# Performance work log

Measured on AMD Instinct MI355X. Metric: run time of the kernel, lower is better.

The kernel has to match this reference:

```python
import jax, jax.numpy as jnp
import numpy as np

EMB, HEADS, LEVELS, POINTS = 256, 8, 4, 4
DHEAD = EMB // HEADS
SHAPES = [(128, 128), (64, 64), (32, 32), (16, 16)]  # (H, W) per level
S = sum(h * w for h, w in SHAPES)  # 21760 flattened multiscale tokens
B, Q = 2, S
LN_EPS = 1e-5


def setup_inputs() -> dict:
    key = jax.random.key(0)
    ks = jax.random.split(key, 10)
    f = lambda k, shp, s=0.02: jax.random.normal(k, shp, jnp.float32) * s
    return {
        "img_feat": jax.random.normal(ks[0], (B, S, EMB), jnp.float32),
        "img_shapes": jnp.array(SHAPES, jnp.int32),
        "img_mask": jnp.zeros((B, S), bool),  # True = padded
        "img_valid_ratios": jnp.ones((B, LEVELS, 2), jnp.float32),
        "query_feat": jax.random.normal(ks[1], (B, Q, EMB), jnp.float32),
        "query_pos": jax.random.normal(ks[2], (B, Q, EMB), jnp.float32),
        "query_points": jax.random.uniform(ks[3], (B, Q, 2), jnp.float32),
        "W_value": f(ks[4], (EMB, EMB)), "b_value": jnp.zeros((EMB,), jnp.float32),
        "W_off": f(ks[5], (EMB, HEADS * LEVELS * POINTS * 2)),
        "b_off": f(ks[6], (HEADS * LEVELS * POINTS * 2,), 0.5),
        "W_attn": f(ks[7], (EMB, HEADS * LEVELS * POINTS)),
        "b_attn": jnp.zeros((HEADS * LEVELS * POINTS,), jnp.float32),
        "W_out": f(ks[8], (EMB, EMB)), "b_out": jnp.zeros((EMB,), jnp.float32),
        "ln_gamma": jnp.ones((EMB,), jnp.float32), "ln_beta": jnp.zeros((EMB,), jnp.float32),
    }


def reference(img_feat, img_shapes, img_mask, img_valid_ratios, query_feat, query_pos,
              query_points, W_value, b_value, W_off, b_off, W_attn, b_attn, W_out, b_out,
              ln_gamma, ln_beta):
    Bq, Qn = query_feat.shape[:2]
    # value projection + padding mask, split heads: [B, S, H, D]
    v = img_feat @ W_value + b_value
    v = jnp.where(img_mask[:, :, None], 0.0, v).reshape(Bq, -1, HEADS, DHEAD)
    q = query_feat + query_pos  # position-modulated query
    off = (q @ W_off + b_off).reshape(Bq, Qn, HEADS, LEVELS, POINTS, 2)
    attn = jax.nn.softmax((q @ W_attn + b_attn).reshape(Bq, Qn, HEADS, LEVELS * POINTS), -1)
    attn = attn.reshape(Bq, Qn, HEADS, LEVELS, POINTS)
    # reference points scaled by per-level valid ratios: [B, Q, L, 2] (x, y in [0,1])
    ref = query_points[:, :, None, :] * img_valid_ratios[:, None, :, :]
    bb = jnp.arange(Bq)[:, None, None, None]
    hh = jnp.arange(HEADS)[None, None, :, None]
    out = jnp.zeros((Bq, Qn, HEADS, DHEAD), q.dtype)
    start = 0
    for l, (H, W) in enumerate(SHAPES):
        norm = jnp.array([W, H], q.dtype)
        loc = ref[:, :, None, l, None, :] + off[:, :, :, l] / norm  # [B,Q,H,P,2]
        # grid_sample align_corners=False pixel coords
        x = loc[..., 0] * W - 0.5
        y = loc[..., 1] * H - 0.5
        x0 = jnp.floor(x); y0 = jnp.floor(y)
        wx = x - x0; wy = y - y0
        x0i = x0.astype(jnp.int32); y0i = y0.astype(jnp.int32)
        samp = jnp.zeros((Bq, Qn, HEADS, POINTS, DHEAD), q.dtype)
        for dx, dy, w in ((0, 0, (1 - wx) * (1 - wy)), (1, 0, wx * (1 - wy)),
                          (0, 1, (1 - wx) * wy), (1, 1, wx * wy)):
            xi = x0i + dx; yi = y0i + dy
            ok = (xi >= 0) & (xi < W) & (yi >= 0) & (yi < H)  # zero padding
            idx = start + jnp.clip(yi, 0, H - 1) * W + jnp.clip(xi, 0, W - 1)
            samp = samp + (w * ok)[..., None] * v[bb, idx, hh, :]
        out = out + jnp.einsum('bqhp,bqhpd->bqhd', attn[:, :, :, l], samp)
        start += H * W
    update = out.reshape(Bq, Qn, EMB) @ W_out + b_out
    # SkipConnection: LayerNorm(skip + dropout(update)), dropout p=0
    x = query_feat + update
    mu = x.mean(-1, keepdims=True)
    var = ((x - mu) ** 2).mean(-1, keepdims=True)
    return (x - mu) * jax.lax.rsqrt(var + LN_EPS) * ln_gamma + ln_beta
```

## Files before the change

kernel.cpp:

```cpp
#include <hip/hip_runtime.h>
#include <hip/hip_bf16.h>

#define EMB 256
#define SEQ 21760
#define NB 2
#define NROW (NB * SEQ)
#define LN_EPS 1e-5f

typedef __hip_bfloat16 bf16;
typedef short bf16x8 __attribute__((ext_vector_type(8)));
typedef float f32x4 __attribute__((ext_vector_type(4)));

__device__ __forceinline__ unsigned short f2bf(float f) {
  __hip_bfloat16 h = __float2bfloat16(f);
  return *reinterpret_cast<unsigned short*>(&h);
}
__device__ __forceinline__ float bf2f(unsigned short u) {
  return __uint_as_float((unsigned int)u << 16);
}
__device__ __forceinline__ float bflo(unsigned int u) { return __uint_as_float(u << 16); }
__device__ __forceinline__ float bfhi(unsigned int u) { return __uint_as_float(u & 0xffff0000u); }

#if defined(__has_builtin)
#if __has_builtin(__builtin_amdgcn_fdot2_f32_bf16)
#define USE_DOT2 1
#endif
#endif
#ifdef USE_DOT2
__device__ __forceinline__ float dot2bf(unsigned int a, unsigned int b, float c) {
  float d;
  asm("v_dot2_f32_bf16 %0, %1, %2, %3" : "=v"(d) : "v"(a), "v"(b), "v"(c));
  return d;
}
#endif

__global__ __launch_bounds__(256) void k_trans_all(const float* __restrict__ Wv,
                                                   const float* __restrict__ Woff,
                                                   const float* __restrict__ Wattn,
                                                   const float* __restrict__ Wout,
                                                   unsigned short* __restrict__ WvT,
                                                   unsigned short* __restrict__ WcatT,
                                                   unsigned short* __restrict__ WoutT) {
  const int bid = blockIdx.x, k = threadIdx.x;
  if (bid < 256) {
    WvT[bid * 256 + k] = f2bf(Wv[k * 256 + bid]);
  } else if (bid < 512) {
    const int n = bid - 256;
    WcatT[n * 256 + k] = f2bf(Woff[k * 256 + n]);
  } else if (bid < 640) {
    const int n = bid - 512;
    WcatT[(256 + n) * 256 + k] = f2bf(Wattn[k * 128 + n]);
  } else {
    const int n = bid - 640;
    WoutT[n * 256 + k] = f2bf(Wout[k * 256 + n]);
  }
}

__global__ __launch_bounds__(256) void k_value(const float* __restrict__ A,
                                               const unsigned short* __restrict__ Wt,
                                               const float* __restrict__ bias,
                                               const unsigned char* __restrict__ mask,
                                               bf16* __restrict__ V) {
  __shared__ unsigned short As[64 * 256];
  const int tid = threadIdx.x;
  const int lane = tid & 63, w = tid >> 6;
  const int row0 = blockIdx.x * 64;
#pragma unroll
  for (int it = 0; it < 8; ++it) {
    const int cid = it * 256 + tid;
    const int row = cid >> 5, c = cid & 31;
    const float4* p = (const float4*)(A + (size_t)(row0 + row) * 256 + c * 8);
    const float4 a0 = p[0], a1 = p[1];
    union { unsigned short u[8]; uint4 q; } pk;
    pk.u[0] = f2bf(a0.x); pk.u[1] = f2bf(a0.y); pk.u[2] = f2bf(a0.z); pk.u[3] = f2bf(a0.w);
    pk.u[4] = f2bf(a1.x); pk.u[5] = f2bf(a1.y); pk.u[6] = f2bf(a1.z); pk.u[7] = f2bf(a1.w);
    *(uint4*)((char*)As + row * 512 + ((c * 16) ^ ((row & 7) << 4))) = pk.q;
  }
  __syncthreads();
  const int lg16 = lane >> 4, l16 = lane & 15;
  f32x4 acc[4][4] = {};
#pragma unroll
  for (int kk = 0; kk < 8; ++kk) {
    bf16x8 af[4], bh[4];
#pragma unroll
    for (int mf = 0; mf < 4; ++mf) {
      const int row = mf * 16 + l16;
      af[mf] = *(const bf16x8*)((const char*)As + row * 512 +
                                ((kk * 64 + lg16 * 16) ^ ((row & 7) << 4)));
    }
#pragma unroll
    for (int nf = 0; nf < 4; ++nf) {
      const int col = w * 64 + nf * 16 + l16;
      bh[nf] = *(const bf16x8*)(Wt + (size_t)col * 256 + kk * 32 + lg16 * 8);
    }
#pragma unroll
    for (int mf = 0; mf < 4; ++mf)
#pragma unroll
      for (int nf = 0; nf < 4; ++nf)
        acc[mf][nf] = __builtin_amdgcn_mfma_f32_16x16x32_bf16(af[mf], bh[nf], acc[mf][nf], 0, 0, 0);
  }
#pragma unroll
  for (int mf = 0; mf < 4; ++mf) {
    const int rbase = mf * 16 + lg16 * 4;
    const uchar4 mk = *(const uchar4*)(mask + row0 + rbase);
#pragma unroll
    for (int nf = 0; nf < 4; ++nf) {
      const int col = w * 64 + nf * 16 + l16;
      const int hh = col >> 5, ch = col & 31;
      const float bb = bias[col];
#pragma unroll
      for (int r = 0; r < 4; ++r) {
        const unsigned char m = (r == 0) ? mk.x : (r == 1) ? mk.y : (r == 2) ? mk.z : mk.w;
        const float v = m ? 0.f : (acc[mf][nf][r] + bb);
        V[(size_t)hh * (NROW * 32) + (size_t)(row0 + rbase + r) * 32 + ch] =
            __float2bfloat16(v);
      }
    }
  }
}

__global__ __launch_bounds__(256) void k_offattn(const float* __restrict__ qf,
                                                 const float* __restrict__ qp,
                                                 const unsigned short* __restrict__ Wt,
                                                 const float* __restrict__ boff,
                                                 const float* __restrict__ battn,
                                                 bf16* __restrict__ off,
                                                 bf16* __restrict__ lg) {
  __shared__ unsigned short As[64 * 256];
  const int tid = threadIdx.x;
  const int lane = tid & 63, w = tid >> 6;
  const int row0 = blockIdx.x * 64;
#pragma unroll
  for (int it = 0; it < 8; ++it) {
    const int cid = it * 256 + tid;
    const int row = cid >> 5, c = cid & 31;
    const float4* pf = (const float4*)(qf + (size_t)(row0 + row) * 256 + c * 8);
    const float4* pp = (const float4*)(qp + (size_t)(row0 + row) * 256 + c * 8);
    const float4 a0 = pf[0], a1 = pf[1], b0 = pp[0], b1 = pp[1];
    union { unsigned short u[8]; uint4 q; } pk;
    pk.u[0] = f2bf(a0.x + b0.x); pk.u[1] = f2bf(a0.y + b0.y);
    pk.u[2] = f2bf(a0.z + b0.z); pk.u[3] = f2bf(a0.w + b0.w);
    pk.u[4] = f2bf(a1.x + b1.x); pk.u[5] = f2bf(a1.y + b1.y);
    pk.u[6] = f2bf(a1.z + b1.z); pk.u[7] = f2bf(a1.w + b1.w);
    *(uint4*)((char*)As + row * 512 + ((c * 16) ^ ((row & 7) << 4))) = pk.q;
  }
  __syncthreads();
  const int lg16 = lane >> 4, l16 = lane & 15;
  f32x4 acc[4][6] = {};
#pragma unroll
  for (int kk = 0; kk < 8; ++kk) {
    bf16x8 af[4], bh[6];
#pragma unroll
    for (int mf = 0; mf < 4; ++mf) {
      const int row = mf * 16 + l16;
      af[mf] = *(const bf16x8*)((const char*)As + row * 512 +
                                ((kk * 64 + lg16 * 16) ^ ((row & 7) << 4)));
    }
#pragma unroll
    for (int nf = 0; nf < 6; ++nf) {
      const int col = w * 96 + nf * 16 + l16;
      bh[nf] = *(const bf16x8*)(Wt + (size_t)col * 256 + kk * 32 + lg16 * 8);
    }
#pragma unroll
    for (int mf = 0; mf < 4; ++mf)
#pragma unroll
      for (int nf = 0; nf < 6; ++nf)
        acc[mf][nf] = __builtin_amdgcn_mfma_f32_16x16x32_bf16(af[mf], bh[nf], acc[mf][nf], 0, 0, 0);
  }
#pragma unroll
  for (int mf = 0; mf < 4; ++mf) {
    const int rbase = row0 + mf * 16 + lg16 * 4;
#pragma unroll
    for (int nf = 0; nf < 6; ++nf) {
      const int col = w * 96 + nf * 16 + l16;
      if (col < 256) {
        const float bb = boff[col];
#pragma unroll
        for (int r = 0; r < 4; ++r)
          off[(size_t)(rbase + r) * 256 + col] = __float2bfloat16(acc[mf][nf][r] + bb);
      } else {
        const float bb = battn[col - 256];
#pragma unroll
        for (int r = 0; r < 4; ++r)
          lg[(size_t)(rbase + r) * 128 + (col - 256)] = __float2bfloat16(acc[mf][nf][r] + bb);
      }
    }
  }
}

__global__ __launch_bounds__(256) void k_sample(const bf16* __restrict__ V,
                                                const bf16* __restrict__ off,
                                                const bf16* __restrict__ lg,
                                                const float* __restrict__ qpts,
                                                const float* __restrict__ vratio,
                                                unsigned short* __restrict__ samp) {
  __shared__ uint4 sIdx[64 * 17];
  __shared__ uint2 sW[64 * 17];
  __shared__ float sMax[64], sInv[64];
  const int t = threadIdx.x;
  const int h = blockIdx.x & 7;
  const int row0 = (blockIdx.x >> 3) * 64;

  if (t < 64) {
    const int row = row0 + t;
    const uint4* lp = (const uint4*)(lg + (size_t)row * 128 + h * 16);
    uint4 u0 = lp[0], u1 = lp[1];
    float v[16];
    v[0] = bflo(u0.x); v[1] = bfhi(u0.x); v[2] = bflo(u0.y); v[3] = bfhi(u0.y);
    v[4] = bflo(u0.z); v[5] = bfhi(u0.z); v[6] = bflo(u0.w); v[7] = bfhi(u0.w);
    v[8] = bflo(u1.x); v[9] = bfhi(u1.x); v[10] = bflo(u1.y); v[11] = bfhi(u1.y);
    v[12] = bflo(u1.z); v[13] = bfhi(u1.z); v[14] = bflo(u1.w); v[15] = bfhi(u1.w);
    float m = v[0];
#pragma unroll
    for (int i = 1; i < 16; ++i) m = fmaxf(m, v[i]);
    float s = 0.f;
#pragma unroll
    for (int i = 0; i < 16; ++i) s += __expf(v[i] - m);
    sMax[t] = m;
    sInv[t] = 1.f / s;
  }
  __syncthreads();

  const int Wl_[4] = {128, 64, 32, 16};
  const int st_[4] = {0, 16384, 20480, 21504};
#pragma unroll
  for (int tt = 0; tt < 4; ++tt) {
    const int sid = t + tt * 256;
    const int q = sid >> 4, i = sid & 15, l = i >> 2;
    const int row = row0 + q;
    const int b = row >= SEQ;
    const unsigned int u = *(const unsigned int*)(off + (size_t)row * 256 + (h * 16 + i) * 2);
    const float ox = bflo(u), oy = bfhi(u);
    const float lgv = bf2f(*(const unsigned short*)(lg + (size_t)row * 128 + h * 16 + i));
    const float e = __expf(lgv - sMax[q]) * sInv[q];
    const float px = qpts[(size_t)row * 2], py = qpts[(size_t)row * 2 + 1];
    const float vrx = vratio[b * 8 + l * 2], vry = vratio[b * 8 + l * 2 + 1];
    const int Wl = Wl_[l];
    const float fW = (float)Wl;
    const float x = fmaf(px * vrx, fW, ox) - 0.5f;
    const float y = fmaf(py * vry, fW, oy) - 0.5f;
    const float fx = floorf(x), fy = floorf(y);
    const float wx = x - fx, wy = y - fy;
    const int x0 = (int)fx, y0 = (int)fy;
    const int x1 = x0 + 1, y1 = y0 + 1;
    const int xc0 = min(max(x0, 0), Wl - 1), xc1 = min(max(x1, 0), Wl - 1);
    const int yc0 = min(max(y0, 0), Wl - 1), yc1 = min(max(y1, 0), Wl - 1);
    const float ox0 = (x0 >= 0 && x0 < Wl) ? e : 0.f;
    const float ox1 = (x1 >= 0 && x1 < Wl) ? e : 0.f;
    const float oy0 = (y0 >= 0 && y0 < Wl) ? 1.f : 0.f;
    const float oy1 = (y1 >= 0 && y1 < Wl) ? 1.f : 0.f;
    const int base = b * SEQ + st_[l];
    const int r0 = base + yc0 * Wl, r1 = base + yc1 * Wl;
    uint4 I4;
    I4.x = (unsigned int)(r0 + xc0) << 6;
    I4.y = (unsigned int)(r0 + xc1) << 6;
    I4.z = (unsigned int)(r1 + xc0) << 6;
    I4.w = (unsigned int)(r1 + xc1) << 6;
    uint2 Wp;
    Wp.x = (unsigned int)f2bf((1.f - wx) * (1.f - wy) * ox0 * oy0) |
           ((unsigned int)f2bf(wx * (1.f - wy) * ox1 * oy0) << 16);
    Wp.y = (unsigned int)f2bf((1.f - wx) * wy * ox0 * oy1) |
           ((unsigned int)f2bf(wx * wy * ox1 * oy1) << 16);
    sIdx[q * 17 + i] = I4;
    sW[q * 17 + i] = Wp;
  }
  __syncthreads();

  const int q = t >> 2, dg = t & 3;
  const int row = row0 + q;
  const char* vbase = (const char*)(V + (size_t)h * (NROW * 32)) + dg * 16;
  float a0 = 0.f, a1 = 0.f, a2 = 0.f, a3 = 0.f;
  float a4 = 0.f, a5 = 0.f, a6 = 0.f, a7 = 0.f;
#pragma unroll
  for (int i = 0; i < 16; ++i) {
    const uint4 I4 = sIdx[q * 17 + i];
    const uint2 Wp = sW[q * 17 + i];
    const uint4 Au = *(const uint4*)(vbase + I4.x);
    const uint4 Bu = *(const uint4*)(vbase + I4.y);
    const uint4 Cu = *(const uint4*)(vbase + I4.z);
    const uint4 Du = *(const uint4*)(vbase + I4.w);
#ifdef USE_DOT2
    a0 = dot2bf(__builtin_amdgcn_perm(Bu.x, Au.x, 0x05040100u), Wp.x, a0);
    a1 = dot2bf(__builtin_amdgcn_perm(Bu.x, Au.x, 0x07060302u), Wp.x, a1);
    a2 = dot2bf(__builtin_amdgcn_perm(Bu.y, Au.y, 0x05040100u), Wp.x, a2);
    a3 = dot2bf(__builtin_amdgcn_perm(Bu.y, Au.y, 0x07060302u), Wp.x, a3);
    a4 = dot2bf(__builtin_amdgcn_perm(Bu.z, Au.z, 0x05040100u), Wp.x, a4);
    a5 = dot2bf(__builtin_amdgcn_perm(Bu.z, Au.z, 0x07060302u), Wp.x, a5);
    a6 = dot2bf(__builtin_amdgcn_perm(Bu.w, Au.w, 0x05040100u), Wp.x, a6);
    a7 = dot2bf(__builtin_amdgcn_perm(Bu.w, Au.w, 0x07060302u), Wp.x, a7);
    a0 = dot2bf(__builtin_amdgcn_perm(Du.x, Cu.x, 0x05040100u), Wp.y, a0);
    a1 = dot2bf(__builtin_amdgcn_perm(Du.x, Cu.x, 0x07060302u), Wp.y, a1);
    a2 = dot2bf(__builtin_amdgcn_perm(Du.y, Cu.y, 0x05040100u), Wp.y, a2);
    a3 = dot2bf(__builtin_amdgcn_perm(Du.y, Cu.y, 0x07060302u), Wp.y, a3);
    a4 = dot2bf(__builtin_amdgcn_perm(Du.z, Cu.z, 0x05040100u), Wp.y, a4);
    a5 = dot2bf(__builtin_amdgcn_perm(Du.z, Cu.z, 0x07060302u), Wp.y, a5);
    a6 = dot2bf(__builtin_amdgcn_perm(Du.w, Cu.w, 0x05040100u), Wp.y, a6);
    a7 = dot2bf(__builtin_amdgcn_perm(Du.w, Cu.w, 0x07060302u), Wp.y, a7);
#else
    {
      const float w0 = bflo(Wp.x), w1 = bfhi(Wp.x);
      const float w2 = bflo(Wp.y), w3 = bfhi(Wp.y);
      a0 = fmaf(w0, bflo(Au.x), a0); a1 = fmaf(w0, bfhi(Au.x), a1);
      a2 = fmaf(w0, bflo(Au.y), a2); a3 = fmaf(w0, bfhi(Au.y), a3);
      a4 = fmaf(w0, bflo(Au.z), a4); a5 = fmaf(w0, bfhi(Au.z), a5);
      a6 = fmaf(w0, bflo(Au.w), a6); a7 = fmaf(w0, bfhi(Au.w), a7);
      a0 = fmaf(w1, bflo(Bu.x), a0); a1 = fmaf(w1, bfhi(Bu.x), a1);
      a2 = fmaf(w1, bflo(Bu.y), a2); a3 = fmaf(w1, bfhi(Bu.y), a3);
      a4 = fmaf(w1, bflo(Bu.z), a4); a5 = fmaf(w1, bfhi(Bu.z), a5);
      a6 = fmaf(w1, bflo(Bu.w), a6); a7 = fmaf(w1, bfhi(Bu.w), a7);
      a0 = fmaf(w2, bflo(Cu.x), a0); a1 = fmaf(w2, bfhi(Cu.x), a1);
      a2 = fmaf(w2, bflo(Cu.y), a2); a3 = fmaf(w2, bfhi(Cu.y), a3);
      a4 = fmaf(w2, bflo(Cu.z), a4); a5 = fmaf(w2, bfhi(Cu.z), a5);
      a6 = fmaf(w2, bflo(Cu.w), a6); a7 = fmaf(w2, bfhi(Cu.w), a7);
      a0 = fmaf(w3, bflo(Du.x), a0); a1 = fmaf(w3, bfhi(Du.x), a1);
      a2 = fmaf(w3, bflo(Du.y), a2); a3 = fmaf(w3, bfhi(Du.y), a3);
      a4 = fmaf(w3, bflo(Du.z), a4); a5 = fmaf(w3, bfhi(Du.z), a5);
      a6 = fmaf(w3, bflo(Du.w), a6); a7 = fmaf(w3, bfhi(Du.w), a7);
    }
#endif
  }
  uint4 pk;
  pk.x = (unsigned int)f2bf(a0) | ((unsigned int)f2bf(a1) << 16);
  pk.y = (unsigned int)f2bf(a2) | ((unsigned int)f2bf(a3) << 16);
  pk.z = (unsigned int)f2bf(a4) | ((unsigned int)f2bf(a5) << 16);
  pk.w = (unsigned int)f2bf(a6) | ((unsigned int)f2bf(a7) << 16);
  *(uint4*)((char*)samp + (size_t)row * 512 + (h * 32 + dg * 8) * 2) = pk;
}

__global__ __launch_bounds__(256) void k_upd(const unsigned short* __restrict__ A,
                                             const unsigned short* __restrict__ Wt,
                                             const float* __restrict__ bias,
                                             bf16* __restrict__ U) {
  __shared__ unsigned short As[64 * 256];
  const int tid = threadIdx.x;
  const int lane = tid & 63, w = tid >> 6;
  const int row0 = blockIdx.x * 64;
#pragma unroll
  for (int it = 0; it < 8; ++it) {
    const int cid = it * 256 + tid;
    const int row = cid >> 5, c = cid & 31;
    const uint4 q = *(const uint4*)(A + (size_t)(row0 + row) * 256 + c * 8);
    *(uint4*)((char*)As + row * 512 + ((c * 16) ^ ((row & 7) << 4))) = q;
  }
  __syncthreads();
  const int lg16 = lane >> 4, l16 = lane & 15;
  f32x4 acc[4][4] = {};
#pragma unroll
  for (int kk = 0; kk < 8; ++kk) {
    bf16x8 af[4], bh[4];
#pragma unroll
    for (int mf = 0; mf < 4; ++mf) {
      const int row = mf * 16 + l16;
      af[mf] = *(const bf16x8*)((const char*)As + row * 512 +
                                ((kk * 64 + lg16 * 16) ^ ((row & 7) << 4)));
    }
#pragma unroll
    for (int nf = 0; nf < 4; ++nf) {
      const int col = w * 64 + nf * 16 + l16;
      bh[nf] = *(const bf16x8*)(Wt + (size_t)col * 256 + kk * 32 + lg16 * 8);
    }
#pragma unroll
    for (int mf = 0; mf < 4; ++mf)
#pragma unroll
      for (int nf = 0; nf < 4; ++nf)
        acc[mf][nf] = __builtin_amdgcn_mfma_f32_16x16x32_bf16(af[mf], bh[nf], acc[mf][nf], 0, 0, 0);
  }
#pragma unroll
  for (int mf = 0; mf < 4; ++mf) {
    const int rbase = row0 + mf * 16 + lg16 * 4;
#pragma unroll
    for (int nf = 0; nf < 4; ++nf) {
      const int col = w * 64 + nf * 16 + l16;
      const float bb = bias[col];
#pragma unroll
      for (int r = 0; r < 4; ++r)
        U[(size_t)(rbase + r) * 256 + col] = __float2bfloat16(acc[mf][nf][r] + bb);
    }
  }
}

__global__ __launch_bounds__(256) void k_ln(const unsigned short* __restrict__ upd,
                                            const float* __restrict__ qf,
                                            const float* __restrict__ gamma,
                                            const float* __restrict__ beta,
                                            float* __restrict__ y) {
  const int w = threadIdx.x >> 6, lane = threadIdx.x & 63;
  const int row = blockIdx.x * 4 + w;
  const int c = lane * 4;
  const ushort4 u = *(const ushort4*)(upd + (size_t)row * 256 + c);
  const float4 qv = *(const float4*)(qf + (size_t)row * 256 + c);
  const float x0 = qv.x + bf2f(u.x);
  const float x1 = qv.y + bf2f(u.y);
  const float x2 = qv.z + bf2f(u.z);
  const float x3 = qv.w + bf2f(u.w);
  float s1 = x0 + x1 + x2 + x3;
  float s2 = x0 * x0 + x1 * x1 + x2 * x2 + x3 * x3;
#pragma unroll
  for (int o = 32; o >= 1; o >>= 1) {
    s1 += __shfl_xor(s1, o);
    s2 += __shfl_xor(s2, o);
  }
  const float mu = s1 * (1.f / 256.f);
  const float var = s2 * (1.f / 256.f) - mu * mu;
  const float rsig = rsqrtf(var + LN_EPS);
  const float4 g = *(const float4*)(gamma + c);
  const float4 bt = *(const float4*)(beta + c);
  float4 o;
  o.x = (x0 - mu) * rsig * g.x + bt.x;
  o.y = (x1 - mu) * rsig * g.y + bt.y;
  o.z = (x2 - mu) * rsig * g.z + bt.z;
  o.w = (x3 - mu) * rsig * g.w + bt.w;
  *(float4*)(y + (size_t)row * 256 + c) = o;
}

extern "C" void kernel_launch(void* const* d_in, const int* in_sizes, int n_in,
                              void* d_out, int out_size, void* d_ws, size_t ws_size,
                              hipStream_t stream) {
  const float* img_feat = (const float*)d_in[0];
  const unsigned char* img_mask = (const unsigned char*)d_in[2];
  const float* vratio = (const float*)d_in[3];
  const float* qf = (const float*)d_in[4];
  const float* qp = (const float*)d_in[5];
  const float* qpts = (const float*)d_in[6];
  const float* Wv = (const float*)d_in[7];
  const float* bv = (const float*)d_in[8];
  const float* Woff = (const float*)d_in[9];
  const float* boff = (const float*)d_in[10];
  const float* Wattn = (const float*)d_in[11];
  const float* battn = (const float*)d_in[12];
  const float* Wout = (const float*)d_in[13];
  const float* bout = (const float*)d_in[14];
  const float* gamma = (const float*)d_in[15];
  const float* beta = (const float*)d_in[16];

  char* ws = (char*)d_ws;
  bf16* V = (bf16*)ws;
  bf16* off = (bf16*)(ws + (size_t)NROW * 256 * 2);
  bf16* lg = (bf16*)(ws + (size_t)NROW * 256 * 4);
  unsigned short* wbase =
      (unsigned short*)(ws + (size_t)NROW * 256 * 4 + (size_t)NROW * 128 * 2);
  unsigned short* WvT = wbase;
  unsigned short* WcatT = WvT + 65536;
  unsigned short* WoutT = WcatT + 98304;

  dim3 blk(256);
  k_trans_all<<<896, blk, 0, stream>>>(Wv, Woff, Wattn, Wout, WvT, WcatT, WoutT);
  k_value<<<NROW / 64, blk, 0, stream>>>(img_feat, WvT, bv, img_mask, V);
  k_offattn<<<NROW / 64, blk, 0, stream>>>(qf, qp, WcatT, boff, battn, off, lg);
  k_sample<<<8 * (NROW / 64), blk, 0, stream>>>(V, off, lg, qpts, vratio,
                                                (unsigned short*)off );
  k_upd<<<NROW / 64, blk, 0, stream>>>((const unsigned short*)off , WoutT,
                                       bout, V );
  k_ln<<<NROW / 4, blk, 0, stream>>>((const unsigned short*)V, qf, gamma, beta,
                                     (float*)d_out);
}
```

Baseline: 177.9 us.

## Fuse output projection with residual add and LayerNorm in one kernel

Merges the output-projection GEMM and the LayerNorm kernel into one kernel. Each wave computes 16 full output rows by swapping the MFMA operands so a row's columns sit in its lanes, then adds bias and residual and does the LayerNorm reduction with two shuffles. This removes the bf16 intermediate write and reread, one kernel launch, and a bf16 rounding of the update. In exchange it drops the shared-memory staging of the A tile and rereads the weight fragments from global/L2 in every wave, and it holds 16 accumulators per lane.

```diff
diff --git a/kernel.cpp b/kernel.cpp
--- a/kernel.cpp
+++ b/kernel.cpp
@@ -327,90 +327,61 @@
   *(uint4*)((char*)samp + (size_t)row * 512 + (h * 32 + dg * 8) * 2) = pk;
 }
 
-__global__ __launch_bounds__(256) void k_upd(const unsigned short* __restrict__ A,
-                                             const unsigned short* __restrict__ Wt,
-                                             const float* __restrict__ bias,
-                                             bf16* __restrict__ U) {
-  __shared__ unsigned short As[64 * 256];
+__global__ __launch_bounds__(256) void k_updln(const unsigned short* __restrict__ samp,
+                                               const unsigned short* __restrict__ Wt,
+                                               const float* __restrict__ bias,
+                                               const float* __restrict__ qf,
+                                               const float* __restrict__ gamma,
+                                               const float* __restrict__ beta,
+                                               float* __restrict__ y) {
   const int tid = threadIdx.x;
   const int lane = tid & 63, w = tid >> 6;
-  const int row0 = blockIdx.x * 64;
-#pragma unroll
-  for (int it = 0; it < 8; ++it) {
-    const int cid = it * 256 + tid;
-    const int row = cid >> 5, c = cid & 31;
-    const uint4 q = *(const uint4*)(A + (size_t)(row0 + row) * 256 + c * 8);
-    *(uint4*)((char*)As + row * 512 + ((c * 16) ^ ((row & 7) << 4))) = q;
-  }
-  __syncthreads();
   const int lg16 = lane >> 4, l16 = lane & 15;
-  f32x4 acc[4][4] = {};
+  const int row = blockIdx.x * 64 + w * 16 + l16;
+  f32x4 acc[16] = {};
 #pragma unroll
   for (int kk = 0; kk < 8; ++kk) {
-    bf16x8 af[4], bh[4];
-#pragma unroll
-    for (int mf = 0; mf < 4; ++mf) {
-      const int row = mf * 16 + l16;
-      af[mf] = *(const bf16x8*)((const char*)As + row * 512 +
-                                ((kk * 64 + lg16 * 16) ^ ((row & 7) << 4)));
-    }
-#pragma unroll
-    for (int nf = 0; nf < 4; ++nf) {
-      const int col = w * 64 + nf * 16 + l16;
-      bh[nf] = *(const bf16x8*)(Wt + (size_t)col * 256 + kk * 32 + lg16 * 8);
-    }
-#pragma unroll
-    for (int mf = 0; mf < 4; ++mf)
-#pragma unroll
-      for (int nf = 0; nf < 4; ++nf)
-        acc[mf][nf] = __builtin_amdgcn_mfma_f32_16x16x32_bf16(af[mf], bh[nf], acc[mf][nf], 0, 0, 0);
-  }
-#pragma unroll
-  for (int mf = 0; mf < 4; ++mf) {
-    const int rbase = row0 + mf * 16 + lg16 * 4;
-#pragma unroll
-    for (int nf = 0; nf < 4; ++nf) {
-      const int col = w * 64 + nf * 16 + l16;
-      const float bb = bias[col];
-#pragma unroll
-      for (int r = 0; r < 4; ++r)
-        U[(size_t)(rbase + r) * 256 + col] = __float2bfloat16(acc[mf][nf][r] + bb);
-    }
-  }
-}
-
-__global__ __launch_bounds__(256) void k_ln(const unsigned short* __restrict__ upd,
-                                            const float* __restrict__ qf,
-                                            const float* __restrict__ gamma,
-                                            const float* __restrict__ beta,
-                                            float* __restrict__ y) {
-  const int w = threadIdx.x >> 6, lane = threadIdx.x & 63;
-  const int row = blockIdx.x * 4 + w;
-  const int c = lane * 4;
-  const ushort4 u = *(const ushort4*)(upd + (size_t)row * 256 + c);
-  const float4 qv = *(const float4*)(qf + (size_t)row * 256 + c);
-  const float x0 = qv.x + bf2f(u.x);
-  const float x1 = qv.y + bf2f(u.y);
-  const float x2 = qv.z + bf2f(u.z);
-  const float x3 = qv.w + bf2f(u.w);
-  float s1 = x0 + x1 + x2 + x3;
-  float s2 = x0 * x0 + x1 * x1 + x2 * x2 + x3 * x3;
-#pragma unroll
-  for (int o = 32; o >= 1; o >>= 1) {
-    s1 += __shfl_xor(s1, o);
-    s2 += __shfl_xor(s2, o);
-  }
+    const bf16x8 bfrag = *(const bf16x8*)(samp + (size_t)row * 256 + kk * 32 + lg16 * 8);
+#pragma unroll
+    for (int mf = 0; mf < 16; ++mf) {
+      const bf16x8 afrag =
+          *(const bf16x8*)(Wt + (size_t)(mf * 16 + l16) * 256 + kk * 32 + lg16 * 8);
+      acc[mf] = __builtin_amdgcn_mfma_f32_16x16x32_bf16(afrag, bfrag, acc[mf], 0, 0, 0);
+    }
+  }
+  float s1 = 0.f, s2 = 0.f;
+#pragma unroll
+  for (int mf = 0; mf < 16; ++mf) {
+    const int c0 = mf * 16 + lg16 * 4;
+    const float4 bb = *(const float4*)(bias + c0);
+    const float4 qv = *(const float4*)(qf + (size_t)row * 256 + c0);
+    acc[mf][0] += bb.x + qv.x;
+    acc[mf][1] += bb.y + qv.y;
+    acc[mf][2] += bb.z + qv.z;
+    acc[mf][3] += bb.w + qv.w;
+#pragma unroll
+    for (int r = 0; r < 4; ++r) {
+      s1 += acc[mf][r];
+      s2 += acc[mf][r] * acc[mf][r];
+    }
+  }
+  s1 += __shfl_xor(s1, 16); s1 += __shfl_xor(s1, 32);
+  s2 += __shfl_xor(s2, 16); s2 += __shfl_xor(s2, 32);
   const float mu = s1 * (1.f / 256.f);
   const float var = s2 * (1.f / 256.f) - mu * mu;
   const float rsig = rsqrtf(var + LN_EPS);
-  const float4 g = *(const float4*)(gamma + c);
-  const float4 bt = *(const float4*)(beta + c);
-  float4 o;
-  o.x = (x0 - mu) * rsig * g.x + bt.x;
-  o.y = (x1 - mu) * rsig * g.y + bt.y;
-  o.z = (x2 - mu) * rsig * g.z + bt.z;
-  o.w = (x3 - mu) * rsig * g.w + bt.w;
-  *(float4*)(y + (size_t)row * 256 + c) = o;
+#pragma unroll
+  for (int mf = 0; mf < 16; ++mf) {
+    const int c0 = mf * 16 + lg16 * 4;
+    const float4 g = *(const float4*)(gamma + c0);
+    const float4 bt = *(const float4*)(beta + c0);
+    float4 o;
+    o.x = (acc[mf][0] - mu) * rsig * g.x + bt.x;
+    o.y = (acc[mf][1] - mu) * rsig * g.y + bt.y;
+    o.z = (acc[mf][2] - mu) * rsig * g.z + bt.z;
+    o.w = (acc[mf][3] - mu) * rsig * g.w + bt.w;
+    *(float4*)(y + (size_t)row * 256 + c0) = o;
+  }
 }
 
 extern "C" void kernel_launch(void* const* d_in, const int* in_sizes, int n_in,
@@ -449,8 +420,6 @@
   k_offattn<<<NROW / 64, blk, 0, stream>>>(qf, qp, WcatT, boff, battn, off, lg);
   k_sample<<<8 * (NROW / 64), blk, 0, stream>>>(V, off, lg, qpts, vratio,
                                                 (unsigned short*)off );
-  k_upd<<<NROW / 64, blk, 0, stream>>>((const unsigned short*)off , WoutT,
-                                       bout, V );
-  k_ln<<<NROW / 4, blk, 0, stream>>>((const unsigned short*)V, qf, gamma, beta,
-                                     (float*)d_out);
-}
+  k_updln<<<NROW / 64, blk, 0, stream>>>((const unsigned short*)off , WoutT,
+                                         bout, qf, gamma, beta, (float*)d_out);
+}
```

Measured after the change: 205.4 us. 15.4% more time.
